# Optimization experiments

Hardware: AMD Instinct MI355X
Metric: run time of the kernel (lower is better)

Reference implementation:

```python
import jax, jax.numpy as jnp
import numpy as np

EPS = 1e-5
B = 32


def _conv(x, w, b, s):
    y = jax.lax.conv_general_dilated(x, w, (s, s), 'VALID',
                                     dimension_numbers=('NCHW', 'OIHW', 'NCHW'))
    return y + b[None, :, None, None]


def _bn(x, g, b):
    # BatchNorm2d in training mode: per-batch statistics over (N,H,W)
    m = jnp.mean(x, axis=(0, 2, 3), keepdims=True)
    v = jnp.var(x, axis=(0, 2, 3), keepdims=True)
    return (x - m) * jax.lax.rsqrt(v + EPS) * g[None, :, None, None] + b[None, :, None, None]


def _pool(x):
    # MaxPool2d(3, stride=2), no padding
    return jax.lax.reduce_window(x, -jnp.inf, jax.lax.max,
                                 (1, 1, 3, 3), (1, 1, 2, 2), 'VALID')


def _backbone(x, p):
    x = _pool(jax.nn.relu(_bn(_conv(x, p['conv1_w'], p['conv1_b'], 2), p['bn1_g'], p['bn1_b'])))
    x = _pool(jax.nn.relu(_bn(_conv(x, p['conv2_w'], p['conv2_b'], 1), p['bn2_g'], p['bn2_b'])))
    x = jax.nn.relu(_bn(_conv(x, p['conv3_w'], p['conv3_b'], 1), p['bn3_g'], p['bn3_b']))
    x = jax.nn.relu(_bn(_conv(x, p['conv4_w'], p['conv4_b'], 1), p['bn4_g'], p['bn4_b']))
    x = _bn(_conv(x, p['conv5_w'], p['conv5_b'], 1), p['bn5_g'], p['bn5_b'])
    return x


def _forward(input1, input2, p):
    o1 = _backbone(input1, p)  # [B, 128, 22, 22]
    o2 = _backbone(input2, p)  # [B, 128, 6, 6]
    b, c, h, w = o1.shape
    # The torch loop sums over batch AND channels at each (i,j), then divides
    # by output2.nelement() (= B*C*6*6). Equivalent: one valid cross-correlation
    # with B*C input channels producing a single [1,1,oH,oW] map, broadcast to B.
    corr = jax.lax.conv_general_dilated(
        o1.reshape(1, b * c, h, w),
        o2.reshape(1, b * c, o2.shape[2], o2.shape[3]),
        (1, 1), 'VALID', dimension_numbers=('NCHW', 'OIHW', 'NCHW'))
    corr = corr / o2.size
    return jnp.broadcast_to(corr, (b, 1, corr.shape[2], corr.shape[3]))


def setup_inputs() -> dict:
    key = jax.random.key(0)
    ks = jax.random.split(key, 8)
    d = {}
    d['input1'] = jax.random.normal(ks[0], (B, 3, 255, 255), jnp.float32)
    d['input2'] = jax.random.normal(ks[1], (B, 3, 127, 127), jnp.float32)
    conv_shapes = {'conv1_w': (96, 3, 11, 11), 'conv2_w': (256, 96, 5, 5),
                   'conv3_w': (192, 256, 3, 3), 'conv4_w': (192, 192, 3, 3),
                   'conv5_w': (128, 192, 3, 3)}
    for i, (name, sh) in enumerate(conv_shapes.items()):
        fan_out = sh[0] * sh[2] * sh[3]  # kaiming_normal_ fan_out, relu gain
        d[name] = jax.random.normal(ks[2 + i], sh, jnp.float32) * np.sqrt(2.0 / fan_out).astype(np.float32)
        d[name.replace('_w', '_b')] = jnp.zeros((sh[0],), jnp.float32)
    for name, c in {'bn1': 96, 'bn2': 256, 'bn3': 192, 'bn4': 192, 'bn5': 128}.items():
        d[name + '_g'] = jnp.ones((c,), jnp.float32)
        d[name + '_b'] = jnp.zeros((c,), jnp.float32)
    return d


def reference(input1, input2, conv1_w, conv1_b, bn1_g, bn1_b,
              conv2_w, conv2_b, bn2_g, bn2_b,
              conv3_w, conv3_b, bn3_g, bn3_b,
              conv4_w, conv4_b, bn4_g, bn4_b,
              conv5_w, conv5_b, bn5_g, bn5_b):
    p = dict(conv1_w=conv1_w, conv1_b=conv1_b, bn1_g=bn1_g, bn1_b=bn1_b,
             conv2_w=conv2_w, conv2_b=conv2_b, bn2_g=bn2_g, bn2_b=bn2_b,
             conv3_w=conv3_w, conv3_b=conv3_b, bn3_g=bn3_g, bn3_b=bn3_b,
             conv4_w=conv4_w, conv4_b=conv4_b, bn4_g=bn4_g, bn4_b=bn4_b,
             conv5_w=conv5_w, conv5_b=conv5_b, bn5_g=bn5_g, bn5_b=bn5_b)
    return _forward(input1, input2, p)
```

## Files before the change

### kernel.cpp

```cpp
#include <hip/hip_runtime.h>
#include <hip/hip_bf16.h>
#include <cstdint>
#include <cstddef>

typedef __attribute__((ext_vector_type(8))) _Float16 f16x8;
typedef __attribute__((ext_vector_type(4))) float f32x4;

__device__ __forceinline__ float h2f(unsigned short u) {
  union { unsigned short s; _Float16 h; } x; x.s = u; return (float)x.h;
}
__device__ __forceinline__ unsigned short f2h(float f) {
  union { unsigned short s; _Float16 h; } x; x.h = (_Float16)f; return x.s;
}
__device__ __forceinline__ void gload_lds16(const void* g, void* l) {
  __builtin_amdgcn_global_load_lds((const __attribute__((address_space(1))) unsigned int*)g,
                                   (__attribute__((address_space(3))) unsigned int*)l, 16, 0, 0);
}
__device__ __forceinline__ int xcd_swz(int bid, int nwg) {
  int q = nwg >> 3, r = nwg & 7;
  int x = bid & 7, idx = bid >> 3;
  return (x < r ? x * (q + 1) : r * (q + 1) + (x - r) * q) + idx;
}

__global__ void in_all(const float* __restrict__ in1, const float* __restrict__ in2,
                       unsigned short* __restrict__ o1, unsigned short* __restrict__ o2) {
  int i = blockIdx.x * 256 + threadIdx.x;
  const int p1 = 32 * 255 * 255;
  const int p2 = 32 * 127 * 127;
  const float* in;
  unsigned short* o;
  int HW;
  if (i < p1) {
    in = in1; o = o1; HW = 255 * 255;
  } else if (i < p1 + p2) {
    i -= p1; in = in2; o = o2; HW = 127 * 127;
  } else return;
  int n = i / HW;
  int r = i - n * HW;
  const float* p = in + (long)n * 3 * HW + r;
  uint2 v;
  v.x = (unsigned)f2h(p[0]) | ((unsigned)f2h(p[HW]) << 16);
  v.y = (unsigned)f2h(p[2 * HW]);
  ((uint2*)o)[i] = v;
}

__device__ __forceinline__ void wtx(const float* __restrict__ w, unsigned short* __restrict__ o,
                                    long i, int Co, int Co_pad, int Ci, int KK) {
  int ci = (int)(i % Ci);
  long r = i / Ci;
  int co = (int)(r % Co_pad);
  int rk = (int)(r / Co_pad);
  float v = 0.f;
  if (co < Co) v = w[((long)co * Ci + ci) * KK + rk];
  o[i] = f2h(v);
}
__global__ void wt_all(const float* __restrict__ w1, const float* __restrict__ w2,
                       const float* __restrict__ w3, const float* __restrict__ w4,
                       const float* __restrict__ w5,
                       unsigned short* __restrict__ W1h, unsigned short* __restrict__ W2,
                       unsigned short* __restrict__ W3, unsigned short* __restrict__ W4,
                       unsigned short* __restrict__ W5) {
  long i = (long)blockIdx.x * 256 + threadIdx.x;
  const long t1 = 17 * 128 * 32;
  const long t2 = 25l * 256 * 96;
  const long t3 = 9l * 192 * 256;
  const long t4 = 9l * 192 * 192;
  const long t5 = 9l * 128 * 192;
  if (i < t1) {
    int j = (int)(i & 31);
    int r = (int)(i >> 5);
    int co = r & 127;
    int kk = r >> 7;
    int run = kk * 4 + (j >> 3);
    int ky = run / 6;
    int e = (run - ky * 6) * 8 + (j & 7);
    int kx = e >> 2, c = e & 3;
    float v = 0.f;
    if (ky < 11 && kx < 11 && c < 3 && co < 96)
      v = w1[((co * 3 + c) * 11 + ky) * 11 + kx];
    W1h[i] = f2h(v);
  } else if (i < t1 + t2) {
    wtx(w2, W2, i - t1, 256, 256, 96, 25);
  } else if (i < t1 + t2 + t3) {
    wtx(w3, W3, i - t1 - t2, 192, 192, 256, 9);
  } else if (i < t1 + t2 + t3 + t4) {
    wtx(w4, W4, i - t1 - t2 - t3, 192, 192, 192, 9);
  } else if (i < t1 + t2 + t3 + t4 + t5) {
    wtx(w5, W5, i - t1 - t2 - t3 - t4, 128, 128, 192, 9);
  }
}

__global__ __launch_bounds__(256, 4)
void conv1_mfma(const unsigned short* __restrict__ in, const unsigned short* __restrict__ wt,
                unsigned short* __restrict__ out, float* __restrict__ part,
                int Hi1, int Ho1, int NPIX1, int BX1, long inOff2, long outOff2,
                int Hi2, int Ho2, int NPIX2) {
  __shared__ __align__(16) unsigned short sA[2][128 * 32];
  __shared__ __align__(16) unsigned short sB[2][128 * 32];
  __shared__ int sOB[128];
  __shared__ float sRed[4][48][2];
  const int t = threadIdx.x;
  const int bxg = xcd_swz(blockIdx.x, gridDim.x);
  const bool br2 = bxg >= BX1;
  const int lbx = br2 ? bxg - BX1 : bxg;
  const unsigned short* inB = in + (br2 ? inOff2 : 0);
  unsigned short* outB = out + (br2 ? outOff2 : 0);
  const int Hi = br2 ? Hi2 : Hi1, Wi = Hi;
  const int Ho = br2 ? Ho2 : Ho1, Wo = Ho;
  const int NPIX = br2 ? NPIX2 : NPIX1;
  const int px0 = lbx * 128;
  if (t < 128) {
    int g = px0 + t;
    int ob = -1;
    if (g < NPIX) {
      int n = g / (Ho * Wo);
      int r = g - n * Ho * Wo;
      int oy = r / Wo, ox = r - (r / Wo) * Wo;
      ob = ((n * Ho + oy) * Wo + ox) * 96;
    }
    sOB[t] = ob;
  }
  long rbase[2];
#pragma unroll
  for (int i = 0; i < 2; ++i) {
    int pxl = i * 64 + (t >> 2);
    int g = px0 + pxl;
    long rb = 0;
    if (g < NPIX) {
      int n = g / (Ho * Wo);
      int r = g - n * Ho * Wo;
      int oy = r / Wo, ox = r - (r / Wo) * Wo;
      rb = ((long)(n * Hi + 2 * oy) * Wi + 2 * ox) * 4;
    }
    rbase[i] = rb;
  }
  const int swz = (t & 3) ^ ((t >> 3) & 3);
  const int W4 = Wi * 4;
  f32x4 acc[4][3];
  f32x4 zz = {0.f, 0.f, 0.f, 0.f};
#pragma unroll
  for (int m = 0; m < 4; ++m)
#pragma unroll
    for (int n = 0; n < 3; ++n) acc[m][n] = zz;
  const int w = t >> 6;
  const int l = t & 63;
  const int wpx = (w & 1) * 64, wco = (w >> 1) * 48;
  const int arow = wpx + (l & 15);
  const int brow = wco + (l & 15);
  const int q8s = (((l >> 4) ^ (((l & 15) >> 1) & 3)) * 8);

  auto stage = [&](int buf, int kk) {
    int run = kk * 4 + swz;
    int ky = run / 6;
    int e0 = (run - ky * 6) * 8;
    long koff = (long)ky * W4 + e0;
    gload_lds16(inB + rbase[0] + koff, &sA[buf][t * 8]);
    gload_lds16(inB + rbase[1] + koff, &sA[buf][(256 + t) * 8]);
    const unsigned short* wp = wt + (long)kk * 4096;
    gload_lds16(wp + (t >> 2) * 32 + swz * 8, &sB[buf][t * 8]);
    if (t < 128)
      gload_lds16(wp + 2048 + (t >> 2) * 32 + swz * 8, &sB[buf][(256 + t) * 8]);
  };

  stage(0, 0);
  __syncthreads();
  int cur = 0;
#pragma unroll 1
  for (int kk = 0; kk < 17; ++kk) {
    if (kk + 1 < 17) stage(cur ^ 1, kk + 1);
    f16x8 av[4], bv[3];
#pragma unroll
    for (int m = 0; m < 4; ++m) av[m] = *(const f16x8*)&sA[cur][(arow + m * 16) * 32 + q8s];
#pragma unroll
    for (int n = 0; n < 3; ++n) bv[n] = *(const f16x8*)&sB[cur][(brow + n * 16) * 32 + q8s];
#pragma unroll
    for (int m = 0; m < 4; ++m)
#pragma unroll
      for (int n = 0; n < 3; ++n)
        acc[m][n] = __builtin_amdgcn_mfma_f32_16x16x32_f16(av[m], bv[n], acc[m][n], 0, 0, 0);
    __syncthreads();
    cur ^= 1;
  }
#pragma unroll
  for (int m = 0; m < 4; ++m) {
#pragma unroll
    for (int r = 0; r < 4; ++r) {
      int pxl = wpx + m * 16 + (l >> 4) * 4 + r;
      int ob = sOB[pxl];
#pragma unroll
      for (int n = 0; n < 3; ++n) {
        int co = wco + n * 16 + (l & 15);
        if (ob >= 0) outB[ob + co] = f2h(acc[m][n][r]);
      }
    }
  }
  float sn[3], qn[3];
#pragma unroll
  for (int n = 0; n < 3; ++n) { sn[n] = 0.f; qn[n] = 0.f; }
#pragma unroll
  for (int m = 0; m < 4; ++m) {
#pragma unroll
    for (int r = 0; r < 4; ++r) {
      int pxl = wpx + m * 16 + (l >> 4) * 4 + r;
      float msk = (px0 + pxl < NPIX) ? 1.f : 0.f;
#pragma unroll
      for (int n = 0; n < 3; ++n) {
        float v = acc[m][n][r] * msk;
        sn[n] += v;
        qn[n] = fmaf(v, v, qn[n]);
      }
    }
  }
#pragma unroll
  for (int n = 0; n < 3; ++n) {
    sn[n] += __shfl_xor(sn[n], 16, 64);
    sn[n] += __shfl_xor(sn[n], 32, 64);
    qn[n] += __shfl_xor(qn[n], 16, 64);
    qn[n] += __shfl_xor(qn[n], 32, 64);
  }
  if (l < 16) {
#pragma unroll
    for (int n = 0; n < 3; ++n) {
      sRed[w][n * 16 + l][0] = sn[n];
      sRed[w][n * 16 + l][1] = qn[n];
    }
  }
  __syncthreads();
  if (t < 96) {
    int g = t / 48;
    int cl = t - g * 48;
    float S = sRed[2 * g][cl][0] + sRed[2 * g + 1][cl][0];
    float Q = sRed[2 * g][cl][1] + sRed[2 * g + 1][cl][1];
    long idx = ((long)t * gridDim.x + bxg) * 2;
    part[idx] = S;
    part[idx + 1] = Q;
  }
}

template <int K, int NB>
__global__ __launch_bounds__(256, 4)
void conv_mfma(const unsigned short* __restrict__ in, const unsigned short* __restrict__ wt,
               unsigned short* __restrict__ out, float* __restrict__ part,
               int Ci, int Co_pad, int Co_real,
               int Hi1, int Ho1, int NPIX1, int BX1, long inOff2, long outOff2,
               int Hi2, int Ho2, int NPIX2) {
  __shared__ __align__(16) unsigned short sA[2][128 * 32];
  __shared__ __align__(16) unsigned short sB[2][128 * 32];
  __shared__ int sOB[128];
  __shared__ float sRed[4][NB * 16][2];
  const int t = threadIdx.x;
  const int bxg = xcd_swz(blockIdx.x, gridDim.x);
  const bool br2 = bxg >= BX1;
  const int lbx = br2 ? bxg - BX1 : bxg;
  const unsigned short* inB = in + (br2 ? inOff2 : 0);
  unsigned short* outB = out + (br2 ? outOff2 : 0);
  const int Hi = br2 ? Hi2 : Hi1, Wi = Hi;
  const int Ho = br2 ? Ho2 : Ho1, Wo = Ho;
  const int NPIX = br2 ? NPIX2 : NPIX1;
  const int px0 = lbx * 128;
  const int co0 = blockIdx.y * (NB * 32);
  if (t < 128) {
    int g = px0 + t;
    int ob = -1;
    if (g < NPIX) {
      int n = g / (Ho * Wo);
      int r = g - n * Ho * Wo;
      int oy = r / Wo, ox = r - (r / Wo) * Wo;
      ob = ((n * Ho + oy) * Wo + ox) * Co_real;
    }
    sOB[t] = ob;
  }
  long rbase[2];
#pragma unroll
  for (int i = 0; i < 2; ++i) {
    int pxl = i * 64 + (t >> 2);
    int g = px0 + pxl;
    long rb = 0;
    if (g < NPIX) {
      int n = g / (Ho * Wo);
      int r = g - n * Ho * Wo;
      int oy = r / Wo, ox = r - (r / Wo) * Wo;
      rb = ((long)(n * Hi + oy) * Wi + ox) * Ci;
    }
    rbase[i] = rb;
  }
  const int seg8 = ((t & 3) ^ ((t >> 3) & 3)) * 8;
  const int colA = t >> 2;
  f32x4 acc[4][NB];
  f32x4 zz = {0.f, 0.f, 0.f, 0.f};
#pragma unroll
  for (int m = 0; m < 4; ++m)
#pragma unroll
    for (int n = 0; n < NB; ++n) acc[m][n] = zz;
  const int w = t >> 6;
  const int l = t & 63;
  const int wpx = (w & 1) * 64, wco = (w >> 1) * (NB * 16);
  const int arow = wpx + (l & 15);
  const int brow = wco + (l & 15);
  const int q8s = (((l >> 4) ^ (((l & 15) >> 1) & 3)) * 8);
  int ci0 = 0, kx = 0, ky = 0;
  const int NK = (Ci >> 5) * K * K;

  auto stage = [&](int buf) {
    long koff = (long)(ky * Wi + kx) * Ci + ci0 + seg8;
    gload_lds16(inB + rbase[0] + koff, &sA[buf][t * 8]);
    gload_lds16(inB + rbase[1] + koff, &sA[buf][(256 + t) * 8]);
    long wbase = (long)((ky * K + kx) * Co_pad + co0) * Ci + ci0 + seg8;
    gload_lds16(wt + wbase + (long)colA * Ci, &sB[buf][t * 8]);
    if (NB == 4 || t < 128)
      gload_lds16(wt + wbase + (long)(64 + colA) * Ci, &sB[buf][(256 + t) * 8]);
    ci0 += 32;
    if (ci0 == Ci) { ci0 = 0; ++kx; if (kx == K) { kx = 0; ++ky; } }
  };

  stage(0);
  __syncthreads();
  int cur = 0;
#pragma unroll 1
  for (int kk = 0; kk < NK; ++kk) {
    if (kk + 1 < NK) stage(cur ^ 1);
    f16x8 av[4], bv[NB];
#pragma unroll
    for (int m = 0; m < 4; ++m) av[m] = *(const f16x8*)&sA[cur][(arow + m * 16) * 32 + q8s];
#pragma unroll
    for (int n = 0; n < NB; ++n) bv[n] = *(const f16x8*)&sB[cur][(brow + n * 16) * 32 + q8s];
#pragma unroll
    for (int m = 0; m < 4; ++m)
#pragma unroll
      for (int n = 0; n < NB; ++n)
        acc[m][n] = __builtin_amdgcn_mfma_f32_16x16x32_f16(av[m], bv[n], acc[m][n], 0, 0, 0);
    __syncthreads();
    cur ^= 1;
  }
#pragma unroll
  for (int m = 0; m < 4; ++m) {
#pragma unroll
    for (int r = 0; r < 4; ++r) {
      int pxl = wpx + m * 16 + (l >> 4) * 4 + r;
      int ob = sOB[pxl];
#pragma unroll
      for (int n = 0; n < NB; ++n) {
        int co = co0 + wco + n * 16 + (l & 15);
        if (ob >= 0 && co < Co_real) outB[ob + co] = f2h(acc[m][n][r]);
      }
    }
  }
  float sn[NB], qn[NB];
#pragma unroll
  for (int n = 0; n < NB; ++n) { sn[n] = 0.f; qn[n] = 0.f; }
#pragma unroll
  for (int m = 0; m < 4; ++m) {
#pragma unroll
    for (int r = 0; r < 4; ++r) {
      int pxl = wpx + m * 16 + (l >> 4) * 4 + r;
      float msk = (px0 + pxl < NPIX) ? 1.f : 0.f;
#pragma unroll
      for (int n = 0; n < NB; ++n) {
        float v = acc[m][n][r] * msk;
        sn[n] += v;
        qn[n] = fmaf(v, v, qn[n]);
      }
    }
  }
#pragma unroll
  for (int n = 0; n < NB; ++n) {
    sn[n] += __shfl_xor(sn[n], 16, 64);
    sn[n] += __shfl_xor(sn[n], 32, 64);
    qn[n] += __shfl_xor(qn[n], 16, 64);
    qn[n] += __shfl_xor(qn[n], 32, 64);
  }
  if (l < 16) {
#pragma unroll
    for (int n = 0; n < NB; ++n) {
      sRed[w][n * 16 + l][0] = sn[n];
      sRed[w][n * 16 + l][1] = qn[n];
    }
  }
  __syncthreads();
  if (t < NB * 32) {
    int g = t / (NB * 16);
    int cl = t - g * (NB * 16);
    float S = sRed[2 * g][cl][0] + sRed[2 * g + 1][cl][0];
    float Q = sRed[2 * g][cl][1] + sRed[2 * g + 1][cl][1];
    long idx = ((long)(co0 + t) * gridDim.x + bxg) * 2;
    part[idx] = S;
    part[idx + 1] = Q;
  }
}

__global__ void bn_finalize(const float* __restrict__ part, const float* __restrict__ g,
                            const float* __restrict__ b, float* __restrict__ sc,
                            float* __restrict__ sh, int C, int BX1, int BXtot,
                            float cnt1, float cnt2) {
  const int cb = blockIdx.x;
  const bool br2 = cb >= C;
  const int c = br2 ? cb - C : cb;
  const int k0 = br2 ? BX1 : 0;
  const int k1 = br2 ? BXtot : BX1;
  const float cnt = br2 ? cnt2 : cnt1;
  const int t = threadIdx.x;
  float s = 0.f, q = 0.f;
  const float* pc = part + (long)c * BXtot * 2;
  for (int k = k0 + t; k < k1; k += 256) {
    s += pc[k * 2];
    q += pc[k * 2 + 1];
  }
  __shared__ float ss[256], qq[256];
  ss[t] = s; qq[t] = q;
  __syncthreads();
  for (int off = 128; off > 0; off >>= 1) {
    if (t < off) { ss[t] += ss[t + off]; qq[t] += qq[t + off]; }
    __syncthreads();
  }
  if (t == 0) {
    float m = ss[0] / cnt;
    float v = qq[0] / cnt - m * m;
    float r = rsqrtf(v + 1e-5f);
    float scl = r * g[c];
    int o = c + (br2 ? 256 : 0);
    sc[o] = scl;
    sh[o] = b[c] - m * scl;
  }
}

template <bool RELU, bool OUTF32>
__global__ void bn_apply_k(const unsigned short* __restrict__ x, void* __restrict__ y,
                           const float* __restrict__ sc, const float* __restrict__ sh,
                           int C, long t81, long t82, long xOff2, long yOff2q4) {
  long i = (long)blockIdx.x * blockDim.x + threadIdx.x;
  if (i >= t81 + t82) return;
  const bool br2 = i >= t81;
  const long ii = br2 ? i - t81 : i;
  const int scO = br2 ? 256 : 0;
  const uint4 v = ((const uint4*)x + (br2 ? xOff2 : 0))[ii];
  int c0 = (int)((ii * 8) % C);
  const float4 s0 = *(const float4*)&sc[scO + c0];
  const float4 s1 = *(const float4*)&sc[scO + c0 + 4];
  const float4 h0 = *(const float4*)&sh[scO + c0];
  const float4 h1 = *(const float4*)&sh[scO + c0 + 4];
  float f[8];
  f[0] = h2f((unsigned short)(v.x & 0xffff)); f[1] = h2f((unsigned short)(v.x >> 16));
  f[2] = h2f((unsigned short)(v.y & 0xffff)); f[3] = h2f((unsigned short)(v.y >> 16));
  f[4] = h2f((unsigned short)(v.z & 0xffff)); f[5] = h2f((unsigned short)(v.z >> 16));
  f[6] = h2f((unsigned short)(v.w & 0xffff)); f[7] = h2f((unsigned short)(v.w >> 16));
  const float S[8] = {s0.x, s0.y, s0.z, s0.w, s1.x, s1.y, s1.z, s1.w};
  const float H[8] = {h0.x, h0.y, h0.z, h0.w, h1.x, h1.y, h1.z, h1.w};
#pragma unroll
  for (int j = 0; j < 8; ++j) {
    f[j] = fmaf(f[j], S[j], H[j]);
    if (RELU) f[j] = fmaxf(f[j], 0.f);
  }
  if (OUTF32) {
    float4* yb = (float4*)y + (br2 ? yOff2q4 : 0);
    float4 o0 = {f[0], f[1], f[2], f[3]}, o1 = {f[4], f[5], f[6], f[7]};
    yb[2 * ii] = o0;
    yb[2 * ii + 1] = o1;
  } else {
    uint4 o;
    o.x = (unsigned)f2h(f[0]) | ((unsigned)f2h(f[1]) << 16);
    o.y = (unsigned)f2h(f[2]) | ((unsigned)f2h(f[3]) << 16);
    o.z = (unsigned)f2h(f[4]) | ((unsigned)f2h(f[5]) << 16);
    o.w = (unsigned)f2h(f[6]) | ((unsigned)f2h(f[7]) << 16);
    ((uint4*)y + (br2 ? xOff2 : 0))[ii] = o;
  }
}

__global__ void bn_pool_k(const unsigned short* __restrict__ in, unsigned short* __restrict__ out,
                          const float* __restrict__ sc, const float* __restrict__ sh,
                          int C8, int Hi1, int Ho1, long t81, long inOff2, long outOff2,
                          int Hi2, int Ho2, long t82) {
  long i = (long)blockIdx.x * blockDim.x + threadIdx.x;
  if (i >= t81 + t82) return;
  const bool br2 = i >= t81;
  const long ii = br2 ? i - t81 : i;
  const int Hi = br2 ? Hi2 : Hi1, Wi = Hi;
  const int Ho = br2 ? Ho2 : Ho1, Wo = Ho;
  const int scO = br2 ? 256 : 0;
  const uint4* inB = (const uint4*)in + (br2 ? inOff2 : 0);
  uint4* outB = (uint4*)out + (br2 ? outOff2 : 0);
  int cg = (int)(ii % C8);
  long r = ii / C8;
  int ox = (int)(r % Wo);
  r /= Wo;
  int oy = (int)(r % Ho);
  int n = (int)(r / Ho);
  const int c0 = cg * 8;
  const float4 s0 = *(const float4*)&sc[scO + c0];
  const float4 s1 = *(const float4*)&sc[scO + c0 + 4];
  const float4 h0 = *(const float4*)&sh[scO + c0];
  const float4 h1 = *(const float4*)&sh[scO + c0 + 4];
  const float S[8] = {s0.x, s0.y, s0.z, s0.w, s1.x, s1.y, s1.z, s1.w};
  const float H[8] = {h0.x, h0.y, h0.z, h0.w, h1.x, h1.y, h1.z, h1.w};
  const uint4* bp = inB + ((long)(n * Hi + 2 * oy) * Wi + 2 * ox) * C8 + cg;
  float m[8];
#pragma unroll
  for (int j = 0; j < 8; ++j) m[j] = -3.4e38f;
#pragma unroll
  for (int dy = 0; dy < 3; ++dy)
#pragma unroll
    for (int dx = 0; dx < 3; ++dx) {
      const uint4 v = bp[((long)dy * Wi + dx) * C8];
      float f[8];
      f[0] = h2f((unsigned short)(v.x & 0xffff)); f[1] = h2f((unsigned short)(v.x >> 16));
      f[2] = h2f((unsigned short)(v.y & 0xffff)); f[3] = h2f((unsigned short)(v.y >> 16));
      f[4] = h2f((unsigned short)(v.z & 0xffff)); f[5] = h2f((unsigned short)(v.z >> 16));
      f[6] = h2f((unsigned short)(v.w & 0xffff)); f[7] = h2f((unsigned short)(v.w >> 16));
#pragma unroll
      for (int j = 0; j < 8; ++j) {
        f[j] = fmaxf(fmaf(f[j], S[j], H[j]), 0.f);
        m[j] = fmaxf(m[j], f[j]);
      }
    }
  uint4 o;
  o.x = (unsigned)f2h(m[0]) | ((unsigned)f2h(m[1]) << 16);
  o.y = (unsigned)f2h(m[2]) | ((unsigned)f2h(m[3]) << 16);
  o.z = (unsigned)f2h(m[4]) | ((unsigned)f2h(m[5]) << 16);
  o.w = (unsigned)f2h(m[6]) | ((unsigned)f2h(m[7]) << 16);
  outB[ii] = o;
}

__global__ void xcorr_part(const float* __restrict__ o1, const float* __restrict__ o2,
                           float* __restrict__ part) {
  const int p = blockIdx.x;
  const int b = blockIdx.y;
  const int oy = p / 17, ox = p - (p / 17) * 17;
  const float* o1b = o1 + (long)b * 22 * 22 * 128;
  const float* o2b = o2 + (long)b * 4608;
  float acc = 0.f;
  for (int i = threadIdx.x; i < 4608; i += 256) {
    int c = i & 127;
    int r = i >> 7;
    int kx = r % 6, ky = r / 6;
    acc = fmaf(o1b[((oy + ky) * 22 + ox + kx) * 128 + c], o2b[i], acc);
  }
#pragma unroll
  for (int off = 32; off > 0; off >>= 1) acc += __shfl_down(acc, off, 64);
  __shared__ float sh[4];
  const int lane = threadIdx.x & 63, wid = threadIdx.x >> 6;
  if (lane == 0) sh[wid] = acc;
  __syncthreads();
  if (threadIdx.x == 0) part[p * 32 + b] = sh[0] + sh[1] + sh[2] + sh[3];
}

__global__ void xcorr_out(const float* __restrict__ part, float* __restrict__ out, int total) {
  int i = blockIdx.x * 256 + threadIdx.x;
  if (i >= total) return;
  int p = i % 289;
  float s = 0.f;
  for (int b = 0; b < 32; ++b) s += part[p * 32 + b];
  out[i] = s * (1.f / 147456.f);
}

extern "C" void kernel_launch(void* const* d_in, const int* in_sizes, int n_in,
                              void* d_out, int out_size, void* d_ws, size_t ws_size,
                              hipStream_t stream) {
  (void)in_sizes; (void)n_in; (void)ws_size; (void)out_size;
  const float* input1 = (const float*)d_in[0];
  const float* input2 = (const float*)d_in[1];
  const float* cw[5];
  const float* bg[5];
  const float* bb[5];
  for (int i = 0; i < 5; ++i) {
    cw[i] = (const float*)d_in[2 + 2 * i];
    bg[i] = (const float*)d_in[12 + 2 * i];
    bb[i] = (const float*)d_in[13 + 2 * i];
  }
  const int H1a = 123, P1a = 61, H2a = 57, P2a = 28, H3a = 26, H4a = 24, H5a = 22;
  const int H1b = 59, P1b = 29, H2b = 25, P2b = 12, H3b = 10, H4b = 8, H5b = 6;
  auto NP = [](int h) { return 32 * h * h; };
  const int NP1a = NP(H1a), NP1b = NP(H1b);
  const int NP2a = NP(H2a), NP2b = NP(H2b);
  const int NP3a = NP(H3a), NP3b = NP(H3b);
  const int NP4a = NP(H4a), NP4b = NP(H4b);
  const int NP5a = NP(H5a), NP5b = NP(H5b);
  auto BX = [](int np) { return (np + 127) / 128; };

  char* p = (char*)d_ws;
  auto alloc = [&](size_t bytes) {
    char* r = p;
    p += (bytes + 255) & ~(size_t)255;
    return r;
  };
  unsigned short* P = (unsigned short*)alloc(((size_t)NP1a + NP1b) * 96 * 2);
  unsigned short* R = (unsigned short*)alloc(((size_t)NP(P1a) + NP(P1b)) * 96 * 2 + 262144);
  unsigned short* Q = (unsigned short*)alloc(((size_t)NP4a + NP4b) * 192 * 2);
  float* O12 = (float*)alloc(((size_t)NP5a + NP5b) * 128 * 4);
  unsigned short* I12h = (unsigned short*)alloc(((size_t)32 * 255 * 255 * 4 + (size_t)32 * 127 * 127 * 4) * 2 + 65536);
  unsigned short* W1h = (unsigned short*)alloc(17l * 128 * 32 * 2);
  unsigned short* W2 = (unsigned short*)alloc(25l * 256 * 96 * 2);
  unsigned short* W3 = (unsigned short*)alloc(9l * 192 * 256 * 2);
  unsigned short* W4 = (unsigned short*)alloc(9l * 192 * 192 * 2);
  unsigned short* W5 = (unsigned short*)alloc(9l * 128 * 192 * 2);
  float* part = (float*)alloc(9000000);
  float* sc = (float*)alloc(512 * 4);
  float* sh = (float*)alloc(512 * 4);
  float* O1 = O12;
  float* O2 = O12 + (size_t)NP5a * 128;

  {
    long wt_tot = 17l * 128 * 32 + 25l * 256 * 96 + 9l * 192 * 256 + 9l * 192 * 192 + 9l * 128 * 192;
    wt_all<<<(unsigned)((wt_tot + 255) / 256), 256, 0, stream>>>(cw[0], cw[1], cw[2], cw[3], cw[4],
                                                                 W1h, W2, W3, W4, W5);
    long in_tot = 32l * 255 * 255 + 32l * 127 * 127;
    in_all<<<(unsigned)((in_tot + 255) / 256), 256, 0, stream>>>(input1, input2, I12h,
                                                                 I12h + 32l * 255 * 255 * 4);
  }

  {
    int BX1 = BX(NP1a), BXt = BX1 + BX(NP1b);
    conv1_mfma<<<(unsigned)BXt, 256, 0, stream>>>(I12h, W1h, P, part,
        255, H1a, NP1a, BX1, 32l * 255 * 255 * 4, (long)NP1a * 96,
        127, H1b, NP1b);
    bn_finalize<<<192, 256, 0, stream>>>(part, bg[0], bb[0], sc, sh, 96, BX1, BXt,
                                         (float)NP1a, (float)NP1b);
    long t81 = (long)NP(P1a) * 96 / 8, t82 = (long)NP(P1b) * 96 / 8;
    bn_pool_k<<<(unsigned)((t81 + t82 + 255) / 256), 256, 0, stream>>>(
        P, R, sc, sh, 12, H1a, P1a, t81, (long)NP1a * 96 / 8, t81, H1b, P1b, t82);
  }
  {
    int BX1 = BX(NP2a), BXt = BX1 + BX(NP2b);
    dim3 g((unsigned)BXt, 2);
    conv_mfma<5, 4><<<g, 256, 0, stream>>>(R, W2, P, part, 96, 256, 256,
        P1a, H2a, NP2a, BX1, (long)NP(P1a) * 96, (long)NP2a * 256,
        P1b, H2b, NP2b);
    bn_finalize<<<512, 256, 0, stream>>>(part, bg[1], bb[1], sc, sh, 256, BX1, BXt,
                                         (float)NP2a, (float)NP2b);
    long t81 = (long)NP(P2a) * 256 / 8, t82 = (long)NP(P2b) * 256 / 8;
    bn_pool_k<<<(unsigned)((t81 + t82 + 255) / 256), 256, 0, stream>>>(
        P, R, sc, sh, 32, H2a, P2a, t81, (long)NP2a * 256 / 8, t81, H2b, P2b, t82);
  }
  {
    int BX1 = BX(NP3a), BXt = BX1 + BX(NP3b);
    dim3 g((unsigned)BXt, 2);
    conv_mfma<3, 3><<<g, 256, 0, stream>>>(R, W3, P, part, 256, 192, 192,
        P2a, H3a, NP3a, BX1, (long)NP(P2a) * 256, (long)NP3a * 192,
        P2b, H3b, NP3b);
    bn_finalize<<<384, 256, 0, stream>>>(part, bg[2], bb[2], sc, sh, 192, BX1, BXt,
                                         (float)NP3a, (float)NP3b);
    long t81 = (long)NP3a * 192 / 8, t82 = (long)NP3b * 192 / 8;
    bn_apply_k<true, false><<<(unsigned)((t81 + t82 + 255) / 256), 256, 0, stream>>>(
        P, P, sc, sh, 192, t81, t82, t81, 0);
  }
  {
    int BX1 = BX(NP4a), BXt = BX1 + BX(NP4b);
    dim3 g((unsigned)BXt, 2);
    conv_mfma<3, 3><<<g, 256, 0, stream>>>(P, W4, Q, part, 192, 192, 192,
        H3a, H4a, NP4a, BX1, (long)NP3a * 192, (long)NP4a * 192,
        H3b, H4b, NP4b);
    bn_finalize<<<384, 256, 0, stream>>>(part, bg[3], bb[3], sc, sh, 192, BX1, BXt,
                                         (float)NP4a, (float)NP4b);
    long t81 = (long)NP4a * 192 / 8, t82 = (long)NP4b * 192 / 8;
    bn_apply_k<true, false><<<(unsigned)((t81 + t82 + 255) / 256), 256, 0, stream>>>(
        Q, Q, sc, sh, 192, t81, t82, t81, 0);
  }
  {
    int BX1 = BX(NP5a), BXt = BX1 + BX(NP5b);
    dim3 g((unsigned)BXt, 1);
    conv_mfma<3, 4><<<g, 256, 0, stream>>>(Q, W5, P, part, 192, 128, 128,
        H4a, H5a, NP5a, BX1, (long)NP4a * 192, (long)NP5a * 128,
        H4b, H5b, NP5b);
    bn_finalize<<<256, 256, 0, stream>>>(part, bg[4], bb[4], sc, sh, 128, BX1, BXt,
                                         (float)NP5a, (float)NP5b);
    long t81 = (long)NP5a * 128 / 8, t82 = (long)NP5b * 128 / 8;
    bn_apply_k<false, true><<<(unsigned)((t81 + t82 + 255) / 256), 256, 0, stream>>>(
        P, O12, sc, sh, 128, t81, t82, t81, (long)NP5a * 128 / 4);
  }

  xcorr_part<<<dim3(289, 32), 256, 0, stream>>>(O1, O2, part);
  xcorr_out<<<(9248 + 255) / 256, 256, 0, stream>>>(part, (float*)d_out, 9248);
}
```

Before: 515.7 us.

## Fuse prep kernels and interleave output-channel blocks for L2 input reuse

Merges the input fp16 conversion and the weight transform into a single prep kernel, removing one launch. In the conv kernels, the 2D grid over (pixel tile, channel half) becomes a 1D grid with both channel halves of a tile adjacent. Adjacent blocks then land on the same XCD via the swizzle and can share the input tile in L2. The partial-sum indexing is updated to use the tile count instead of gridDim.x.

```diff
diff --git a/kernel.cpp b/kernel.cpp
--- a/kernel.cpp
+++ b/kernel.cpp
@@ -20,28 +20,6 @@
   int q = nwg >> 3, r = nwg & 7;
   int x = bid & 7, idx = bid >> 3;
   return (x < r ? x * (q + 1) : r * (q + 1) + (x - r) * q) + idx;
-}
-
-__global__ void in_all(const float* __restrict__ in1, const float* __restrict__ in2,
-                       unsigned short* __restrict__ o1, unsigned short* __restrict__ o2) {
-  int i = blockIdx.x * 256 + threadIdx.x;
-  const int p1 = 32 * 255 * 255;
-  const int p2 = 32 * 127 * 127;
-  const float* in;
-  unsigned short* o;
-  int HW;
-  if (i < p1) {
-    in = in1; o = o1; HW = 255 * 255;
-  } else if (i < p1 + p2) {
-    i -= p1; in = in2; o = o2; HW = 127 * 127;
-  } else return;
-  int n = i / HW;
-  int r = i - n * HW;
-  const float* p = in + (long)n * 3 * HW + r;
-  uint2 v;
-  v.x = (unsigned)f2h(p[0]) | ((unsigned)f2h(p[HW]) << 16);
-  v.y = (unsigned)f2h(p[2 * HW]);
-  ((uint2*)o)[i] = v;
 }
 
 __device__ __forceinline__ void wtx(const float* __restrict__ w, unsigned short* __restrict__ o,
@@ -54,13 +32,37 @@
   if (co < Co) v = w[((long)co * Ci + ci) * KK + rk];
   o[i] = f2h(v);
 }
-__global__ void wt_all(const float* __restrict__ w1, const float* __restrict__ w2,
-                       const float* __restrict__ w3, const float* __restrict__ w4,
-                       const float* __restrict__ w5,
-                       unsigned short* __restrict__ W1h, unsigned short* __restrict__ W2,
-                       unsigned short* __restrict__ W3, unsigned short* __restrict__ W4,
-                       unsigned short* __restrict__ W5) {
-  long i = (long)blockIdx.x * 256 + threadIdx.x;
+__global__ void prep_all(const float* __restrict__ in1, const float* __restrict__ in2,
+                         unsigned short* __restrict__ o1, unsigned short* __restrict__ o2,
+                         const float* __restrict__ w1, const float* __restrict__ w2,
+                         const float* __restrict__ w3, const float* __restrict__ w4,
+                         const float* __restrict__ w5,
+                         unsigned short* __restrict__ W1h, unsigned short* __restrict__ W2,
+                         unsigned short* __restrict__ W3, unsigned short* __restrict__ W4,
+                         unsigned short* __restrict__ W5) {
+  long gi = (long)blockIdx.x * 256 + threadIdx.x;
+  const long p1 = 32l * 255 * 255;
+  const long p2 = 32l * 127 * 127;
+  if (gi < p1 + p2) {
+    const float* in;
+    unsigned short* o;
+    int HW;
+    long i = gi;
+    if (i < p1) {
+      in = in1; o = o1; HW = 255 * 255;
+    } else {
+      i -= p1; in = in2; o = o2; HW = 127 * 127;
+    }
+    int n = (int)(i / HW);
+    int r = (int)(i - (long)n * HW);
+    const float* p = in + (long)n * 3 * HW + r;
+    uint2 v;
+    v.x = (unsigned)f2h(p[0]) | ((unsigned)f2h(p[HW]) << 16);
+    v.y = (unsigned)f2h(p[2 * HW]);
+    ((uint2*)o)[i] = v;
+    return;
+  }
+  long i = gi - (p1 + p2);
   const long t1 = 17 * 128 * 32;
   const long t2 = 25l * 256 * 96;
   const long t3 = 9l * 192 * 256;
@@ -237,7 +239,7 @@
   }
 }
 
-template <int K, int NB>
+template <int K, int NB, int NCO>
 __global__ __launch_bounds__(256, 4)
 void conv_mfma(const unsigned short* __restrict__ in, const unsigned short* __restrict__ wt,
                unsigned short* __restrict__ out, float* __restrict__ part,
@@ -249,7 +251,11 @@
   __shared__ int sOB[128];
   __shared__ float sRed[4][NB * 16][2];
   const int t = threadIdx.x;
-  const int bxg = xcd_swz(blockIdx.x, gridDim.x);
+  const int nT = gridDim.x / NCO;
+  int tile, coid;
+  if (NCO == 2) { tile = blockIdx.x >> 1; coid = blockIdx.x & 1; }
+  else { tile = blockIdx.x; coid = 0; }
+  const int bxg = xcd_swz(tile, nT);
   const bool br2 = bxg >= BX1;
   const int lbx = br2 ? bxg - BX1 : bxg;
   const unsigned short* inB = in + (br2 ? inOff2 : 0);
@@ -258,7 +264,7 @@
   const int Ho = br2 ? Ho2 : Ho1, Wo = Ho;
   const int NPIX = br2 ? NPIX2 : NPIX1;
   const int px0 = lbx * 128;
-  const int co0 = blockIdx.y * (NB * 32);
+  const int co0 = coid * (NB * 32);
   if (t < 128) {
     int g = px0 + t;
     int ob = -1;
@@ -382,7 +388,7 @@
     int cl = t - g * (NB * 16);
     float S = sRed[2 * g][cl][0] + sRed[2 * g + 1][cl][0];
     float Q = sRed[2 * g][cl][1] + sRed[2 * g + 1][cl][1];
-    long idx = ((long)(co0 + t) * gridDim.x + bxg) * 2;
+    long idx = ((long)(co0 + t) * nT + bxg) * 2;
     part[idx] = S;
     part[idx + 1] = Q;
   }
@@ -598,12 +604,12 @@
   float* O2 = O12 + (size_t)NP5a * 128;
 
   {
+    long in_tot = 32l * 255 * 255 + 32l * 127 * 127;
     long wt_tot = 17l * 128 * 32 + 25l * 256 * 96 + 9l * 192 * 256 + 9l * 192 * 192 + 9l * 128 * 192;
-    wt_all<<<(unsigned)((wt_tot + 255) / 256), 256, 0, stream>>>(cw[0], cw[1], cw[2], cw[3], cw[4],
-                                                                 W1h, W2, W3, W4, W5);
-    long in_tot = 32l * 255 * 255 + 32l * 127 * 127;
-    in_all<<<(unsigned)((in_tot + 255) / 256), 256, 0, stream>>>(input1, input2, I12h,
-                                                                 I12h + 32l * 255 * 255 * 4);
+    long tot = in_tot + wt_tot;
+    prep_all<<<(unsigned)((tot + 255) / 256), 256, 0, stream>>>(
+        input1, input2, I12h, I12h + 32l * 255 * 255 * 4,
+        cw[0], cw[1], cw[2], cw[3], cw[4], W1h, W2, W3, W4, W5);
   }
 
   {
@@ -619,8 +625,7 @@
   }
   {
     int BX1 = BX(NP2a), BXt = BX1 + BX(NP2b);
-    dim3 g((unsigned)BXt, 2);
-    conv_mfma<5, 4><<<g, 256, 0, stream>>>(R, W2, P, part, 96, 256, 256,
+    conv_mfma<5, 4, 2><<<(unsigned)(BXt * 2), 256, 0, stream>>>(R, W2, P, part, 96, 256, 256,
         P1a, H2a, NP2a, BX1, (long)NP(P1a) * 96, (long)NP2a * 256,
         P1b, H2b, NP2b);
     bn_finalize<<<512, 256, 0, stream>>>(part, bg[1], bb[1], sc, sh, 256, BX1, BXt,
@@ -631,8 +636,7 @@
   }
   {
     int BX1 = BX(NP3a), BXt = BX1 + BX(NP3b);
-    dim3 g((unsigned)BXt, 2);
-    conv_mfma<3, 3><<<g, 256, 0, stream>>>(R, W3, P, part, 256, 192, 192,
+    conv_mfma<3, 3, 2><<<(unsigned)(BXt * 2), 256, 0, stream>>>(R, W3, P, part, 256, 192, 192,
         P2a, H3a, NP3a, BX1, (long)NP(P2a) * 256, (long)NP3a * 192,
         P2b, H3b, NP3b);
     bn_finalize<<<384, 256, 0, stream>>>(part, bg[2], bb[2], sc, sh, 192, BX1, BXt,
@@ -643,8 +647,7 @@
   }
   {
     int BX1 = BX(NP4a), BXt = BX1 + BX(NP4b);
-    dim3 g((unsigned)BXt, 2);
-    conv_mfma<3, 3><<<g, 256, 0, stream>>>(P, W4, Q, part, 192, 192, 192,
+    conv_mfma<3, 3, 2><<<(unsigned)(BXt * 2), 256, 0, stream>>>(P, W4, Q, part, 192, 192, 192,
         H3a, H4a, NP4a, BX1, (long)NP3a * 192, (long)NP4a * 192,
         H3b, H4b, NP4b);
     bn_finalize<<<384, 256, 0, stream>>>(part, bg[3], bb[3], sc, sh, 192, BX1, BXt,
@@ -655,8 +658,7 @@
   }
   {
     int BX1 = BX(NP5a), BXt = BX1 + BX(NP5b);
-    dim3 g((unsigned)BXt, 1);
-    conv_mfma<3, 4><<<g, 256, 0, stream>>>(Q, W5, P, part, 192, 128, 128,
+    conv_mfma<3, 4, 1><<<(unsigned)BXt, 256, 0, stream>>>(Q, W5, P, part, 192, 128, 128,
         H4a, H5a, NP5a, BX1, (long)NP4a * 192, (long)NP5a * 128,
         H4b, H5b, NP5b);
     bn_finalize<<<256, 256, 0, stream>>>(part, bg[4], bb[4], sc, sh, 128, BX1, BXt,
```

After: 508.0 us, median of 2. Within noise of the previous version (-1.5%).
